# Kernel tuning notes

Hardware: AMD Instinct MI355X
Metric: run time of the kernel (lower is better)

## Reference

```python
import jax, jax.numpy as jnp
import numpy as np

N_HEAD = 16
D_MODEL = 1024
D_HEAD = 64
B = 2
S = 2048      # query length
M = 512       # memory length
K = S + M     # key length
L = 2 * K - 1 # relative position table length
SCALE = 1.0 / np.sqrt(D_MODEL)  # NOTE: module scales by 1/sqrt(d_model), not d_head
EPS = 1e-5


def layer_norm(x, gamma, beta):
    mu = jnp.mean(x, axis=-1, keepdims=True)
    var = jnp.mean(jnp.square(x - mu), axis=-1, keepdims=True)
    return (x - mu) * jax.lax.rsqrt(var + EPS) * gamma + beta


def skew(qpos, mem_len):
    # qpos: (B, H, S, 2K-1) -> relative-position scores aligned to keys (B, H, S, K)
    b, h, s, l = qpos.shape
    k_len = (l + 1) // 2
    pad = jnp.full((b, h, s, 1), -jnp.inf, dtype=qpos.dtype)
    rel = jnp.concatenate([qpos, pad], axis=-1)          # (B,H,S,2K)
    rel = rel.reshape(b, h, s * (l + 1))[..., : s * l]    # drop tail, shift rows
    rel = rel.reshape(b, h, s, l)
    start = (k_len - 1) - mem_len
    return rel[..., start : start + k_len]


def setup_inputs() -> dict:
    key = jax.random.key(0)
    ks = jax.random.split(key, 8)
    w_scale = 1.0 / np.sqrt(D_MODEL)
    hidden = jax.random.normal(ks[0], (B, S, D_MODEL), jnp.float32)
    memory = jax.random.normal(ks[1], (B, M, D_MODEL), jnp.float32)
    pos_emb = jax.random.normal(ks[2], (B, L, D_HEAD), jnp.float32)
    Wq = jax.random.normal(ks[3], (D_MODEL, N_HEAD * D_HEAD), jnp.float32) * w_scale
    Wk = jax.random.normal(ks[4], (D_MODEL, N_HEAD * D_HEAD), jnp.float32) * w_scale
    Wv = jax.random.normal(ks[5], (D_MODEL, N_HEAD * D_HEAD), jnp.float32) * w_scale
    Wo = jax.random.normal(ks[6], (N_HEAD * D_HEAD, D_MODEL), jnp.float32) * w_scale
    gamma = jnp.ones((D_MODEL,), jnp.float32)
    beta = jnp.zeros((D_MODEL,), jnp.float32)
    # causal mask with memory: query i may attend keys j <= i + M; True = drop
    i = jnp.arange(S)[:, None]
    j = jnp.arange(K)[None, :]
    mask = j > (i + M)  # (S, K) bool
    return {"hidden": hidden, "pos_emb": pos_emb, "memory": memory,
            "Wq": Wq, "Wk": Wk, "Wv": Wv, "Wo": Wo,
            "gamma": gamma, "beta": beta, "mask": mask}


def reference(hidden, pos_emb, memory, Wq, Wk, Wv, Wo, gamma, beta, mask):
    combined = jnp.concatenate([memory, hidden], axis=1)  # (B, K, D)
    hn = layer_norm(hidden, gamma, beta)                  # pre_lnorm
    cn = layer_norm(combined, gamma, beta)
    q = (hn @ Wq).reshape(B, S, N_HEAD, D_HEAD).transpose(0, 2, 1, 3)  # (B,H,S,Dh)
    k = (cn @ Wk).reshape(B, K, N_HEAD, D_HEAD).transpose(0, 2, 1, 3)  # (B,H,K,Dh)
    v = (cn @ Wv).reshape(B, K, N_HEAD, D_HEAD).transpose(0, 2, 1, 3)  # (B,H,K,Dh)
    scores = jnp.einsum("bhsd,bhkd->bhsk", q, k)           # content term
    qpos = jnp.einsum("bhsd,bld->bhsl", q, pos_emb)        # position term (B,H,S,2K-1)
    scores = (scores + skew(qpos, M)) * SCALE
    scores = jnp.where(mask[None, None], -jnp.inf, scores)
    attn = jax.nn.softmax(scores, axis=-1)
    atten_vec = jnp.einsum("bhsk,bhkd->bshd", attn, v).reshape(B, S, N_HEAD * D_HEAD)
    output = atten_vec @ Wo
    # faithful quirk: residual uses the layer-normed hidden when pre_lnorm=True
    return hn + output
```

## Files before the change

### kernel.cpp

```cpp
#include <hip/hip_runtime.h>

typedef unsigned short u16;
typedef float f32x4 __attribute__((ext_vector_type(4)));
typedef short short8 __attribute__((ext_vector_type(8)));

#define MFMA_BF16(a, b, c) __builtin_amdgcn_mfma_f32_16x16x32_bf16((a), (b), (c), 0, 0, 0)

#define NEG_BIG (-30000.0f)

__device__ __forceinline__ float bf2f(u16 v) {
  union { unsigned int u; float f; } c; c.u = ((unsigned int)v) << 16; return c.f;
}
__device__ __forceinline__ u16 f2bf(float f) {
  union { float f; unsigned int u; } c; c.f = f;
  return (u16)((c.u + 0x7fffu + ((c.u >> 16) & 1u)) >> 16);
}

__global__ __launch_bounds__(256) void cast_pe_k(const float* __restrict__ src, u16* __restrict__ dst, int n4) {
  const int idx = blockIdx.x * 256 + threadIdx.x;
  if (idx >= n4) return;
  const float4 d = *(const float4*)&src[idx * 4];
  ushort4 o;
  o.x = f2bf(d.x); o.y = f2bf(d.y); o.z = f2bf(d.z); o.w = f2bf(d.w);
  *(ushort4*)&dst[idx * 4] = o;
}

__global__ __launch_bounds__(256) void transpose_k(const float* __restrict__ W0, const float* __restrict__ W1,
                                                   const float* __restrict__ W2, const float* __restrict__ W3,
                                                   u16* __restrict__ Wt) {
  __shared__ float t[32][33];
  const float* W = (blockIdx.z == 0) ? W0 : (blockIdx.z == 1) ? W1 : (blockIdx.z == 2) ? W2 : W3;
  u16* dst = Wt + (size_t)blockIdx.z * 1024 * 1024;
  const int tx = threadIdx.x, ty = threadIdx.y;
  const int x0 = blockIdx.x * 32, y0 = blockIdx.y * 32;
#pragma unroll
  for (int i = 0; i < 32; i += 8)
    t[ty + i][tx] = W[(size_t)(y0 + ty + i) * 1024 + x0 + tx];
  __syncthreads();
#pragma unroll
  for (int i = 0; i < 32; i += 8)
    dst[(size_t)(x0 + ty + i) * 1024 + y0 + tx] = f2bf(t[tx][ty + i]);
}

__global__ __launch_bounds__(256) void ln_k(const float* __restrict__ hid, const float* __restrict__ mem,
                                            const float* __restrict__ gam, const float* __restrict__ bet,
                                            u16* __restrict__ cn) {
  const int row = blockIdx.x;
  const int b = (row >= 2560) ? 1 : 0;
  const int r = row - b * 2560;
  const float* src = (r < 512) ? (mem + ((size_t)b * 512 + r) * 1024)
                               : (hid + ((size_t)b * 2048 + (r - 512)) * 1024);
  const int tid = threadIdx.x;
  const float4 d = *(const float4*)&src[tid * 4];
  float x[4] = {d.x, d.y, d.z, d.w};
  float s = x[0] + x[1] + x[2] + x[3];
  float q = x[0]*x[0] + x[1]*x[1] + x[2]*x[2] + x[3]*x[3];
#pragma unroll
  for (int o = 1; o < 64; o <<= 1) { s += __shfl_xor(s, o); q += __shfl_xor(q, o); }
  __shared__ float sb[4], qsb[4];
  const int wave = tid >> 6;
  if ((tid & 63) == 0) { sb[wave] = s; qsb[wave] = q; }
  __syncthreads();
  s = sb[0] + sb[1] + sb[2] + sb[3];
  q = qsb[0] + qsb[1] + qsb[2] + qsb[3];
  const float mu = s * (1.0f / 1024.0f);
  const float var = q * (1.0f / 1024.0f) - mu * mu;
  const float rstd = rsqrtf(fmaxf(var, 0.0f) + 1e-5f);
  u16 o4[4];
#pragma unroll
  for (int i = 0; i < 4; ++i) {
    const int c = tid * 4 + i;
    o4[i] = f2bf((x[i] - mu) * rstd * gam[c] + bet[c]);
  }
  uint2 pk;
  pk.x = (unsigned)o4[0] | ((unsigned)o4[1] << 16);
  pk.y = (unsigned)o4[2] | ((unsigned)o4[3] << 16);
  *(uint2*)&cn[((size_t)b * 2560 + r) * 1024 + tid * 4] = pk;
}

template <int MODE>
__global__ __launch_bounds__(256) void gemm_k(const u16* __restrict__ A, const u16* __restrict__ Bt,
                                              u16* __restrict__ qb, u16* __restrict__ kbo,
                                              u16* __restrict__ vtb, float* __restrict__ outf,
                                              const u16* __restrict__ resid) {
  __shared__ u16 As[2][64][40];
  __shared__ u16 Bs[2][64][40];
  const int tid = threadIdx.x;
  const int lane = tid & 63, wave = tid >> 6;
  const int quad = lane >> 4, l15 = lane & 15;
  const int row0 = blockIdx.y * 64, col0 = blockIdx.x * 64;
  const int sr = tid >> 2, sc8 = (tid & 3) * 8;
  const u16* ga = A + (size_t)(row0 + sr) * 1024 + sc8;
  const u16* gb = Bt + (size_t)(col0 + sr) * 1024 + sc8;
  f32x4 z = {0.f, 0.f, 0.f, 0.f};
  f32x4 acc[4];
#pragma unroll
  for (int i = 0; i < 4; ++i) acc[i] = z;
  *(uint4*)&As[0][sr][sc8] = *(const uint4*)ga;
  *(uint4*)&Bs[0][sr][sc8] = *(const uint4*)gb;
  __syncthreads();
  for (int it = 0; it < 32; ++it) {
    const int cur = it & 1;
    const int kn = (it + 1 < 32) ? (it + 1) * 32 : it * 32;
    const uint4 ua = *(const uint4*)(ga + kn);
    const uint4 ub = *(const uint4*)(gb + kn);
    const short8 af = *(const short8*)&As[cur][16 * wave + l15][quad * 8];
#pragma unroll
    for (int n = 0; n < 4; ++n)
      acc[n] = MFMA_BF16(af, *(const short8*)&Bs[cur][16 * n + l15][quad * 8], acc[n]);
    *(uint4*)&As[cur ^ 1][sr][sc8] = ua;
    *(uint4*)&Bs[cur ^ 1][sr][sc8] = ub;
    __syncthreads();
  }
#pragma unroll
  for (int n = 0; n < 4; ++n) {
#pragma unroll
    for (int r = 0; r < 4; ++r) {
      const int R = row0 + 16 * wave + quad * 4 + r;
      const int C = col0 + 16 * n + l15;
      const float v = acc[n][r];
      if (MODE == 0) {
        const int nc = col0 >> 10;
        const int c = C & 1023, h = c >> 6, dh = c & 63;
        const int b = (R >= 2560) ? 1 : 0, kk = R - b * 2560;
        if (nc == 0) {
          if (kk >= 512)
            qb[(((size_t)(b * 16 + h)) * 2048 + (kk - 512)) * 64 + dh] = f2bf(v * 0.03125f);
        } else if (nc == 1) {
          kbo[(((size_t)(b * 16 + h)) * 2560 + kk) * 64 + dh] = f2bf(v);
        } else {
          vtb[(((size_t)(b * 16 + h)) * 64 + dh) * 2560 + kk] = f2bf(v);
        }
      } else {
        const size_t rrow = (size_t)(R >> 11) * 2560 + 512 + (R & 2047);
        outf[(size_t)R * 1024 + C] = v + bf2f(resid[rrow * 1024 + C]);
      }
    }
  }
}

__global__ __launch_bounds__(512, 4) void attn_k(const u16* __restrict__ q, const u16* __restrict__ kb,
                                                 const u16* __restrict__ vt, const u16* __restrict__ pe,
                                                 u16* __restrict__ av) {
  __shared__ u16 Kt[2][64][72];
  __shared__ u16 Vt[2][64][72];
  __shared__ u16 Pw[8][16][68];
  const int tid = threadIdx.x, lane = tid & 63, wave = tid >> 6;
  const int quad = lane >> 4, l15 = lane & 15;
  const int bh = blockIdx.y, b = bh >> 4, h = bh & 15;
  const int qt = (blockIdx.y < 16) ? (15 - blockIdx.x) : blockIdx.x;
  const int i0 = qt * 128;
  const int qi0 = i0 + wave * 16;
  const u16* qrow = q + ((size_t)bh * 2048 + qi0 + l15) * 64 + quad * 8;
  const short8 aq0 = *(const short8*)qrow;
  const short8 aq1 = *(const short8*)(qrow + 32);
  const u16* pp = pe + ((long)b * 5119 - qi0 + 2032 + l15) * 64 + quad * 8;
  const int sr = tid >> 3, sc8 = (tid & 7) * 8;
  f32x4 z = {0.f, 0.f, 0.f, 0.f};
  f32x4 acc[4];
#pragma unroll
  for (int i = 0; i < 4; ++i) acc[i] = z;
  float lrow[4] = {0.f, 0.f, 0.f, 0.f};
  const int ntiles = 2 * qt + 10;
  const int jlast = qi0 + 527;
  *(uint4*)&Kt[0][sr][sc8] = *(const uint4*)&kb[((size_t)bh * 2560 + sr) * 64 + sc8];
  *(uint4*)&Vt[0][sr][sc8] = *(const uint4*)&vt[((size_t)bh * 64 + sr) * 2560 + sc8];
  __syncthreads();
  for (int jt = 0; jt < ntiles; ++jt) {
    const int j0 = jt * 64;
    const int cur = jt & 1;
    const int jn = (jt + 1 < ntiles) ? (jt + 1) : jt;
    const uint4 ku = *(const uint4*)&kb[((size_t)bh * 2560 + jn * 64 + sr) * 64 + sc8];
    const uint4 vu = *(const uint4*)&vt[((size_t)bh * 64 + sr) * 2560 + jn * 64 + sc8];
    if (j0 <= jlast) {
      short8 pb[5], pb2[5];
#pragma unroll
      for (int g = 0; g < 5; ++g) {
        pb[g]  = *(const short8*)(pp + 1024 * g);
        pb2[g] = *(const short8*)(pp + 1024 * g + 32);
      }
      f32x4 sc[4];
#pragma unroll
      for (int s = 0; s < 4; ++s) {
        sc[s] = MFMA_BF16(aq0, *(const short8*)&Kt[cur][16 * s + l15][quad * 8], z);
        sc[s] = MFMA_BF16(aq1, *(const short8*)&Kt[cur][16 * s + l15][32 + quad * 8], sc[s]);
      }
      f32x4 qp[5];
#pragma unroll
      for (int g = 0; g < 5; ++g) {
        qp[g] = MFMA_BF16(aq0, pb[g], z);
        qp[g] = MFMA_BF16(aq1, pb2[g], qp[g]);
      }
#pragma unroll
      for (int r = 0; r < 4; ++r) {
        const int di = quad * 4 + r;
        const int o = l15 - di + 15;
        const int src = quad * 16 + (o & 15);
        const float g0 = __shfl(qp[0][r], src);
        const float g1 = __shfl(qp[1][r], src);
        const float g2 = __shfl(qp[2][r], src);
        const float g3 = __shfl(qp[3][r], src);
        const float g4 = __shfl(qp[4][r], src);
        const bool lo = (o < 16);
        float s0 = sc[0][r] + (lo ? g0 : g1);
        float s1 = sc[1][r] + (lo ? g1 : g2);
        float s2 = sc[2][r] + (lo ? g2 : g3);
        float s3 = sc[3][r] + (lo ? g3 : g4);
        const int jlim = qi0 + di + 512 - j0 - l15;
        if (0 > jlim)  s0 = NEG_BIG;
        if (16 > jlim) s1 = NEG_BIG;
        if (32 > jlim) s2 = NEG_BIG;
        if (48 > jlim) s3 = NEG_BIG;
        const float p0 = __expf(s0);
        const float p1 = __expf(s1);
        const float p2 = __expf(s2);
        const float p3 = __expf(s3);
        lrow[r] += (p0 + p1) + (p2 + p3);
        Pw[wave][di][l15]      = f2bf(p0);
        Pw[wave][di][16 + l15] = f2bf(p1);
        Pw[wave][di][32 + l15] = f2bf(p2);
        Pw[wave][di][48 + l15] = f2bf(p3);
      }
      asm volatile("s_waitcnt lgkmcnt(0)" ::: "memory");
      const short8 pf0 = *(const short8*)&Pw[wave][l15][quad * 8];
      const short8 pf1 = *(const short8*)&Pw[wave][l15][32 + quad * 8];
#pragma unroll
      for (int n = 0; n < 4; ++n) {
        acc[n] = MFMA_BF16(pf0, *(const short8*)&Vt[cur][16 * n + l15][quad * 8], acc[n]);
        acc[n] = MFMA_BF16(pf1, *(const short8*)&Vt[cur][16 * n + l15][32 + quad * 8], acc[n]);
      }
    }
    *(uint4*)&Kt[cur ^ 1][sr][sc8] = ku;
    *(uint4*)&Vt[cur ^ 1][sr][sc8] = vu;
    __syncthreads();
    pp += 4096;
  }
#pragma unroll
  for (int r = 0; r < 4; ++r) {
    float lsum = lrow[r];
#pragma unroll
    for (int o = 1; o < 16; o <<= 1) lsum += __shfl_xor(lsum, o);
    const float inv = 1.0f / lsum;
    const int s = qi0 + quad * 4 + r;
#pragma unroll
    for (int n = 0; n < 4; ++n) {
      const int c = h * 64 + n * 16 + l15;
      av[((size_t)b * 2048 + s) * 1024 + c] = f2bf(acc[n][r] * inv);
    }
  }
}

extern "C" void kernel_launch(void* const* d_in, const int* in_sizes, int n_in,
                              void* d_out, int out_size, void* d_ws, size_t ws_size,
                              hipStream_t stream) {
  const float* hidden = (const float*)d_in[0];
  const float* pe     = (const float*)d_in[1];
  const float* memv   = (const float*)d_in[2];
  const float* Wq     = (const float*)d_in[3];
  const float* Wk     = (const float*)d_in[4];
  const float* Wv     = (const float*)d_in[5];
  const float* Wo     = (const float*)d_in[6];
  const float* gam    = (const float*)d_in[7];
  const float* bet    = (const float*)d_in[8];

  u16* ws  = (u16*)d_ws;
  u16* cn  = ws;
  u16* qb  = cn  + (size_t)5120 * 1024;
  u16* kb  = qb  + (size_t)4096 * 1024;
  u16* vt  = kb  + (size_t)5120 * 1024;
  u16* av  = vt  + (size_t)5120 * 1024;
  u16* wt  = av  + (size_t)4096 * 1024;
  u16* peb = wt  + (size_t)4 * 1024 * 1024;

  const int pe_n4 = (2 * 5119 * 64) / 4;
  cast_pe_k<<<(pe_n4 + 255) / 256, 256, 0, stream>>>(pe, peb, pe_n4);
  ln_k<<<5120, 256, 0, stream>>>(hidden, memv, gam, bet, cn);
  transpose_k<<<dim3(32, 32, 4), dim3(32, 8), 0, stream>>>(Wq, Wk, Wv, Wo, wt);
  gemm_k<0><<<dim3(48, 80), 256, 0, stream>>>(cn, wt, qb, kb, vt, nullptr, nullptr);
  attn_k<<<dim3(16, 32), 512, 0, stream>>>(qb, kb, vt, peb, av);
  gemm_k<1><<<dim3(16, 64), 256, 0, stream>>>(av, wt + (size_t)3 * 1024 * 1024,
                                              nullptr, nullptr, nullptr, (float*)d_out, cn);
}
```

Measured before the change: 378.1 us.

## Use 128x128 tiled QKV GEMM with direct global-to-LDS loads and swizzle

Replaces the 64x64 QKV projection GEMM with a 128x128 tile kernel where each wave computes a 64x64 sub-tile and K steps by 64. Global data goes straight into LDS through global_load_lds, and an XOR swizzle on the LDS columns avoids bank conflicts. The aim is more operand reuse per byte loaded and less register staging, which should lower memory traffic for the largest GEMM. The new kernel drops double buffering, so loads and MFMAs are not overlapped within a block, and it relies on occupancy to hide that latency. The output GEMM is split into its own non-templated kernel.

```diff
diff --git a/kernel.cpp b/kernel.cpp
--- a/kernel.cpp
+++ b/kernel.cpp
@@ -7,6 +7,9 @@
 #define MFMA_BF16(a, b, c) __builtin_amdgcn_mfma_f32_16x16x32_bf16((a), (b), (c), 0, 0, 0)
 
 #define NEG_BIG (-30000.0f)
+
+typedef __attribute__((address_space(1))) const void gas_void;
+typedef __attribute__((address_space(3))) void las_void;
 
 __device__ __forceinline__ float bf2f(u16 v) {
   union { unsigned int u; float f; } c; c.u = ((unsigned int)v) << 16; return c.f;
@@ -78,11 +81,84 @@
   *(uint2*)&cn[((size_t)b * 2560 + r) * 1024 + tid * 4] = pk;
 }
 
-template <int MODE>
-__global__ __launch_bounds__(256) void gemm_k(const u16* __restrict__ A, const u16* __restrict__ Bt,
-                                              u16* __restrict__ qb, u16* __restrict__ kbo,
-                                              u16* __restrict__ vtb, float* __restrict__ outf,
-                                              const u16* __restrict__ resid) {
+__global__ __launch_bounds__(256, 3) void gemm128_k(const u16* __restrict__ A, const u16* __restrict__ Bt,
+                                                    u16* __restrict__ qb, u16* __restrict__ kbo,
+                                                    u16* __restrict__ vtb) {
+  __shared__ u16 As[128][64];
+  __shared__ u16 Bs[128][64];
+  const int tid = threadIdx.x;
+  const int lane = tid & 63, w = tid >> 6;
+  const int quad = lane >> 4, l15 = lane & 15, r7 = l15 & 7;
+  const int wr = w >> 1, wc = w & 1;
+  const int row0 = blockIdx.y * 128, col0 = blockIdx.x * 128;
+  const int rloc = w * 8 + (lane >> 3);
+  const int cg = ((lane & 7) ^ ((lane >> 3) & 7)) * 8;
+  const u16* ga = A + (size_t)(row0 + rloc) * 1024 + cg;
+  const u16* gb = Bt + (size_t)(col0 + rloc) * 1024 + cg;
+  f32x4 z = {0.f, 0.f, 0.f, 0.f};
+  f32x4 acc[4][4];
+#pragma unroll
+  for (int m = 0; m < 4; ++m)
+#pragma unroll
+    for (int n = 0; n < 4; ++n) acc[m][n] = z;
+  for (int kt = 0; kt < 16; ++kt) {
+    const int k0 = kt * 64;
+#pragma unroll
+    for (int g2 = 0; g2 < 4; ++g2) {
+      __builtin_amdgcn_global_load_lds((gas_void*)(ga + (size_t)g2 * 32 * 1024 + k0),
+                                       (las_void*)(&As[g2 * 32 + w * 8][0]), 16, 0, 0);
+      __builtin_amdgcn_global_load_lds((gas_void*)(gb + (size_t)g2 * 32 * 1024 + k0),
+                                       (las_void*)(&Bs[g2 * 32 + w * 8][0]), 16, 0, 0);
+    }
+    __syncthreads();
+    short8 af0[4], af1[4];
+#pragma unroll
+    for (int m = 0; m < 4; ++m) {
+      const int row = wr * 64 + m * 16 + l15;
+      af0[m] = *(const short8*)&As[row][(quad ^ r7) * 8];
+      af1[m] = *(const short8*)&As[row][((quad + 4) ^ r7) * 8];
+    }
+#pragma unroll
+    for (int n = 0; n < 4; ++n) {
+      const int row = wc * 64 + n * 16 + l15;
+      const short8 bf0 = *(const short8*)&Bs[row][(quad ^ r7) * 8];
+      const short8 bf1 = *(const short8*)&Bs[row][((quad + 4) ^ r7) * 8];
+#pragma unroll
+      for (int m = 0; m < 4; ++m) {
+        acc[m][n] = MFMA_BF16(af0[m], bf0, acc[m][n]);
+        acc[m][n] = MFMA_BF16(af1[m], bf1, acc[m][n]);
+      }
+    }
+    __syncthreads();
+  }
+  const int nc = col0 >> 10;
+#pragma unroll
+  for (int m = 0; m < 4; ++m) {
+#pragma unroll
+    for (int n = 0; n < 4; ++n) {
+#pragma unroll
+      for (int r = 0; r < 4; ++r) {
+        const int R = row0 + wr * 64 + m * 16 + quad * 4 + r;
+        const int C = col0 + wc * 64 + n * 16 + l15;
+        const float v = acc[m][n][r];
+        const int c = C & 1023, h = c >> 6, dh = c & 63;
+        const int b = (R >= 2560) ? 1 : 0, kk = R - b * 2560;
+        if (nc == 0) {
+          if (kk >= 512)
+            qb[(((size_t)(b * 16 + h)) * 2048 + (kk - 512)) * 64 + dh] = f2bf(v * 0.03125f);
+        } else if (nc == 1) {
+          kbo[(((size_t)(b * 16 + h)) * 2560 + kk) * 64 + dh] = f2bf(v);
+        } else {
+          vtb[(((size_t)(b * 16 + h)) * 64 + dh) * 2560 + kk] = f2bf(v);
+        }
+      }
+    }
+  }
+}
+
+__global__ __launch_bounds__(256) void gemm_out_k(const u16* __restrict__ A, const u16* __restrict__ Bt,
+                                                  float* __restrict__ outf,
+                                                  const u16* __restrict__ resid) {
   __shared__ u16 As[2][64][40];
   __shared__ u16 Bs[2][64][40];
   const int tid = threadIdx.x;
@@ -118,23 +194,8 @@
     for (int r = 0; r < 4; ++r) {
       const int R = row0 + 16 * wave + quad * 4 + r;
       const int C = col0 + 16 * n + l15;
-      const float v = acc[n][r];
-      if (MODE == 0) {
-        const int nc = col0 >> 10;
-        const int c = C & 1023, h = c >> 6, dh = c & 63;
-        const int b = (R >= 2560) ? 1 : 0, kk = R - b * 2560;
-        if (nc == 0) {
-          if (kk >= 512)
-            qb[(((size_t)(b * 16 + h)) * 2048 + (kk - 512)) * 64 + dh] = f2bf(v * 0.03125f);
-        } else if (nc == 1) {
-          kbo[(((size_t)(b * 16 + h)) * 2560 + kk) * 64 + dh] = f2bf(v);
-        } else {
-          vtb[(((size_t)(b * 16 + h)) * 64 + dh) * 2560 + kk] = f2bf(v);
-        }
-      } else {
-        const size_t rrow = (size_t)(R >> 11) * 2560 + 512 + (R & 2047);
-        outf[(size_t)R * 1024 + C] = v + bf2f(resid[rrow * 1024 + C]);
-      }
+      const size_t rrow = (size_t)(R >> 11) * 2560 + 512 + (R & 2047);
+      outf[(size_t)R * 1024 + C] = acc[n][r] + bf2f(resid[rrow * 1024 + C]);
     }
   }
 }
@@ -276,8 +337,8 @@
   cast_pe_k<<<(pe_n4 + 255) / 256, 256, 0, stream>>>(pe, peb, pe_n4);
   ln_k<<<5120, 256, 0, stream>>>(hidden, memv, gam, bet, cn);
   transpose_k<<<dim3(32, 32, 4), dim3(32, 8), 0, stream>>>(Wq, Wk, Wv, Wo, wt);
-  gemm_k<0><<<dim3(48, 80), 256, 0, stream>>>(cn, wt, qb, kb, vt, nullptr, nullptr);
+  gemm128_k<<<dim3(24, 40), 256, 0, stream>>>(cn, wt, qb, kb, vt);
   attn_k<<<dim3(16, 32), 512, 0, stream>>>(qb, kb, vt, peb, av);
-  gemm_k<1><<<dim3(16, 64), 256, 0, stream>>>(av, wt + (size_t)3 * 1024 * 1024,
-                                              nullptr, nullptr, nullptr, (float*)d_out, cn);
-}
+  gemm_out_k<<<dim3(16, 64), 256, 0, stream>>>(av, wt + (size_t)3 * 1024 * 1024,
+                                               (float*)d_out, cn);
+}
```

After: 357.4 us. -5.5%, faster.
